# Performance work log

Hardware: AMD Instinct MI355X
Metric: run time of the kernel (lower is better)

Reference implementation:

```python
import jax, jax.numpy as jnp
import numpy as np

D_MODEL = 1024
NUM_HEADS = 16
D_K = D_MODEL // NUM_HEADS
B, L = 2, 4096


def setup_inputs() -> dict:
    key = jax.random.key(0)
    ks = jax.random.split(key, 12)
    s = 0.02
    return {
        "q": jax.random.normal(ks[0], (B, L, D_MODEL), dtype=jnp.float32),
        "k": jax.random.normal(ks[1], (B, L, D_MODEL), dtype=jnp.float32),
        "v": jax.random.normal(ks[2], (B, L, D_MODEL), dtype=jnp.float32),
        "Wq": jax.random.normal(ks[3], (D_MODEL, D_MODEL), dtype=jnp.float32) * s,
        "bq": jax.random.normal(ks[4], (D_MODEL,), dtype=jnp.float32) * s,
        "Wk": jax.random.normal(ks[5], (D_MODEL, D_MODEL), dtype=jnp.float32) * s,
        "bk": jax.random.normal(ks[6], (D_MODEL,), dtype=jnp.float32) * s,
        "Wv": jax.random.normal(ks[7], (D_MODEL, D_MODEL), dtype=jnp.float32) * s,
        "bv": jax.random.normal(ks[8], (D_MODEL,), dtype=jnp.float32) * s,
        "Wo": jax.random.normal(ks[9], (D_MODEL, D_MODEL), dtype=jnp.float32) * s,
        "bo": jax.random.normal(ks[10], (D_MODEL,), dtype=jnp.float32) * s,
    }


def reference(q, k, v, Wq, bq, Wk, bk, Wv, bv, Wo, bo):
    b, l, _ = q.shape
    # projections (torch Linear: x @ W.T + b), reshape to [b, l, h, d]
    qf = (q @ Wq.T + bq).reshape(b, l, NUM_HEADS, D_K)
    kf = (k @ Wk.T + bk).reshape(b, l, NUM_HEADS, D_K)
    vf = (v @ Wv.T + bv).reshape(b, l, NUM_HEADS, D_K)
    # elu+1 feature map (positive features)
    qf = jax.nn.elu(qf) + 1.0
    kf = jax.nn.elu(kf) + 1.0
    # normalizer uses full-sequence k sum (as in the original code)
    z = 1.0 / (jnp.einsum("blhd,bhd->blh", qf, kf.sum(axis=1)) + 1e-6)
    # cumulative sums over sequence (the linear-attention scan state)
    k_cum = jnp.cumsum(kf, axis=1)  # [b, l, h, d]
    v_cum = jnp.cumsum(vf, axis=1)  # [b, l, h, d]
    context = jnp.einsum("blhd,blhd->blh", qf, k_cum)  # [b, l, h]
    context = context[..., None] * v_cum * z[..., None]  # [b, l, h, d]
    context = context.reshape(b, l, NUM_HEADS * D_K)
    return context @ Wo.T + bo
```

## Files before the change

### kernel.cpp

```cpp
#include <hip/hip_runtime.h>
#include <hip/hip_bf16.h>
#include <cstdint>
#include <cstddef>

#define D_MODEL 1024
#define NUM_HEADS 16
#define DK_DIM 64
#define BATCH 2
#define SEQ 4096
#define MROWS (BATCH*SEQ)
#define NCHUNK 128
#define CHUNK 32

#define BM 256
#define BN 128
#define BK 64
#define NSLOT 3
#define SLOT_SH (BM*BK + BN*BK)
#define KTILES (D_MODEL/BK)

typedef __attribute__((ext_vector_type(4))) float f32x4;
typedef __attribute__((ext_vector_type(2))) float f32x2;
typedef __attribute__((ext_vector_type(8))) short bf16x8;
typedef __attribute__((ext_vector_type(4))) short s16x4;

__device__ __forceinline__ float b2f(short s) {
  union { uint32_t u; float f; } c; c.u = ((uint32_t)(uint16_t)s) << 16; return c.f;
}
__device__ __forceinline__ short f2b(float f) {
  union { float f; uint32_t u; } c; c.f = f;
  uint32_t u = c.u;
  u += 0x7FFFu + ((u >> 16) & 1u);
  return (short)(u >> 16);
}
__device__ __forceinline__ f32x4 b4_to_f4(s16x4 s) {
  f32x4 r;
  r.x = b2f(s.x); r.y = b2f(s.y); r.z = b2f(s.z); r.w = b2f(s.w);
  return r;
}

__global__ __launch_bounds__(256) void cvt_f32_bf16(const float* __restrict__ in,
                                                    short* __restrict__ out, int n4) {
  int i = blockIdx.x * 256 + threadIdx.x;
  if (i >= n4) return;
  float4 v = reinterpret_cast<const float4*>(in)[i];
  s16x4 o;
  o.x = f2b(v.x); o.y = f2b(v.y); o.z = f2b(v.z); o.w = f2b(v.w);
  reinterpret_cast<s16x4*>(out)[i] = o;
}

__global__ __launch_bounds__(256) void cvt_w4(
    const float* __restrict__ s0, const float* __restrict__ s1,
    const float* __restrict__ s2, const float* __restrict__ s3,
    short* __restrict__ dst) {
  const int y = blockIdx.y;
  const float* s = (y == 0) ? s0 : (y == 1) ? s1 : (y == 2) ? s2 : s3;
  const int i = blockIdx.x * 256 + threadIdx.x;
  float4 v = reinterpret_cast<const float4*>(s)[i];
  s16x4 o;
  o.x = f2b(v.x); o.y = f2b(v.y); o.z = f2b(v.z); o.w = f2b(v.w);
  reinterpret_cast<s16x4*>(dst)[(size_t)y * (D_MODEL * D_MODEL / 4) + i] = o;
}

template<int OUTBF16>
__global__ __launch_bounds__(512, 2) void gemm8(
    const short* __restrict__ A, const short* __restrict__ Bw,
    const float* __restrict__ bias, void* __restrict__ Cout, int act)
{
  extern __shared__ __align__(16) short lds[];
  const int tid = threadIdx.x;
  const int wid = tid >> 6;
  const int lane = tid & 63;
  const int brow = blockIdx.x * BM;
  const int bcol = blockIdx.y * BN;
  const int wr = wid >> 1, wc = wid & 1;

  f32x4 acc[4][4];
#pragma unroll
  for (int i = 0; i < 4; ++i)
#pragma unroll
    for (int j = 0; j < 4; ++j)
#pragma unroll
      for (int t = 0; t < 4; ++t) acc[i][j][t] = 0.f;

  const int srow = lane >> 3;
  const int sgel = ((lane & 7) ^ srow) * 8;

  auto stage = [&](int t) {
    short* sA = lds + (t % NSLOT) * SLOT_SH;
    short* sB = sA + BM * BK;
    const int k0 = t * BK;
#pragma unroll
    for (int i = 0; i < 4; ++i) {
      const int r = i * 64 + wid * 8;
      const short* g = A + (size_t)(brow + r + srow) * D_MODEL + k0 + sgel;
      __builtin_amdgcn_global_load_lds((const __attribute__((address_space(1))) void*)g,
          (__attribute__((address_space(3))) void*)(sA + r * BK), 16, 0, 0);
    }
#pragma unroll
    for (int i = 0; i < 2; ++i) {
      const int r = i * 64 + wid * 8;
      const short* g = Bw + (size_t)(bcol + r + srow) * D_MODEL + k0 + sgel;
      __builtin_amdgcn_global_load_lds((const __attribute__((address_space(1))) void*)g,
          (__attribute__((address_space(3))) void*)(sB + r * BK), 16, 0, 0);
    }
  };

  stage(0);
  stage(1);

  const int lane15 = lane & 15;
  const int swz = (lane & 7) << 4;
  const int kq = (lane >> 4) * 16;

  for (int t = 0; t < KTILES; ++t) {
    if (t == KTILES - 1) { asm volatile("s_waitcnt vmcnt(0)" ::: "memory"); }
    else                 { asm volatile("s_waitcnt vmcnt(6)" ::: "memory"); }
    __builtin_amdgcn_s_barrier();
    __builtin_amdgcn_sched_barrier(0);
    if (t + 2 < KTILES) stage(t + 2);

    const char* sAb = (const char*)(lds + (t % NSLOT) * SLOT_SH);
    const char* sBb = sAb + BM * BK * 2;

    auto rdA = [&](int mi, int ks) -> bf16x8 {
      const int row = wr * 64 + mi * 16 + lane15;
      const int off = row * 128 + (((ks * 64 + kq)) ^ swz);
      return *reinterpret_cast<const bf16x8*>(sAb + off);
    };
    auto rdB = [&](int nj, int ks) -> bf16x8 {
      const int row = wc * 64 + nj * 16 + lane15;
      const int off = row * 128 + (((ks * 64 + kq)) ^ swz);
      return *reinterpret_cast<const bf16x8*>(sBb + off);
    };

    bf16x8 Af[2][2], Bf[2][2][2];

#pragma unroll
    for (int m2 = 0; m2 < 2; ++m2)
#pragma unroll
      for (int ks = 0; ks < 2; ++ks) Af[m2][ks] = rdA(m2, ks);
#pragma unroll
    for (int j2 = 0; j2 < 2; ++j2)
#pragma unroll
      for (int ks = 0; ks < 2; ++ks) Bf[0][j2][ks] = rdB(j2, ks);
    __builtin_amdgcn_s_setprio(1);
#pragma unroll
    for (int m2 = 0; m2 < 2; ++m2)
#pragma unroll
      for (int j2 = 0; j2 < 2; ++j2)
#pragma unroll
        for (int ks = 0; ks < 2; ++ks)
          acc[m2][j2] = __builtin_amdgcn_mfma_f32_16x16x32_bf16(Af[m2][ks], Bf[0][j2][ks], acc[m2][j2], 0, 0, 0);
    __builtin_amdgcn_s_setprio(0);
    __builtin_amdgcn_sched_barrier(0);

#pragma unroll
    for (int j2 = 0; j2 < 2; ++j2)
#pragma unroll
      for (int ks = 0; ks < 2; ++ks) Bf[1][j2][ks] = rdB(2 + j2, ks);
    __builtin_amdgcn_s_setprio(1);
#pragma unroll
    for (int m2 = 0; m2 < 2; ++m2)
#pragma unroll
      for (int j2 = 0; j2 < 2; ++j2)
#pragma unroll
        for (int ks = 0; ks < 2; ++ks)
          acc[m2][2 + j2] = __builtin_amdgcn_mfma_f32_16x16x32_bf16(Af[m2][ks], Bf[1][j2][ks], acc[m2][2 + j2], 0, 0, 0);
    __builtin_amdgcn_s_setprio(0);
    __builtin_amdgcn_sched_barrier(0);

#pragma unroll
    for (int m2 = 0; m2 < 2; ++m2)
#pragma unroll
      for (int ks = 0; ks < 2; ++ks) Af[m2][ks] = rdA(2 + m2, ks);
    __builtin_amdgcn_s_setprio(1);
#pragma unroll
    for (int m2 = 0; m2 < 2; ++m2)
#pragma unroll
      for (int j2 = 0; j2 < 2; ++j2)
#pragma unroll
        for (int ks = 0; ks < 2; ++ks)
          acc[2 + m2][2 + j2] = __builtin_amdgcn_mfma_f32_16x16x32_bf16(Af[m2][ks], Bf[1][j2][ks], acc[2 + m2][2 + j2], 0, 0, 0);
    __builtin_amdgcn_s_setprio(0);
    __builtin_amdgcn_sched_barrier(0);

    __builtin_amdgcn_s_setprio(1);
#pragma unroll
    for (int m2 = 0; m2 < 2; ++m2)
#pragma unroll
      for (int j2 = 0; j2 < 2; ++j2)
#pragma unroll
        for (int ks = 0; ks < 2; ++ks)
          acc[2 + m2][j2] = __builtin_amdgcn_mfma_f32_16x16x32_bf16(Af[m2][ks], Bf[0][j2][ks], acc[2 + m2][j2], 0, 0, 0);
    __builtin_amdgcn_s_setprio(0);
    __builtin_amdgcn_sched_barrier(0);
  }

  const int rsub = (lane >> 4) * 4;
#pragma unroll
  for (int nj = 0; nj < 4; ++nj) {
    const int col = bcol + wc * 64 + nj * 16 + lane15;
    const float bv = bias[col];
#pragma unroll
    for (int mi = 0; mi < 4; ++mi) {
#pragma unroll
      for (int tt = 0; tt < 4; ++tt) {
        const int row = brow + wr * 64 + mi * 16 + rsub + tt;
        float v = acc[mi][nj][tt] + bv;
        if (act) v = (v > 0.f) ? (v + 1.f) : __expf(v);
        if (OUTBF16) ((short*)Cout)[(size_t)row * D_MODEL + col] = f2b(v);
        else ((float*)Cout)[(size_t)row * D_MODEL + col] = v;
      }
    }
  }
}

__global__ __launch_bounds__(256) void chunk_sums(
    const short* __restrict__ kf, const short* __restrict__ vf,
    float* __restrict__ ck, float* __restrict__ cv)
{
  const int gw = blockIdx.x * 4 + (threadIdx.x >> 6);
  const int lane = threadIdx.x & 63;
  const int c = gw & (NCHUNK - 1);
  const int h = (gw >> 7) & (NUM_HEADS - 1);
  const int b = gw >> 11;
  const int half = lane >> 5;
  const int dpair = (lane & 31) * 2;
  const size_t base = ((size_t)(b * SEQ + c * CHUNK) * NUM_HEADS + h) * DK_DIM + dpair;

  float skx = 0.f, sky = 0.f, svx = 0.f, svy = 0.f;
#pragma unroll
  for (int i = 0; i < CHUNK / 2; ++i) {
    const size_t off = base + (size_t)(2 * i + half) * D_MODEL;
    uint32_t ku = *reinterpret_cast<const uint32_t*>(&kf[off]);
    uint32_t vu = *reinterpret_cast<const uint32_t*>(&vf[off]);
    skx += b2f((short)(ku & 0xffff)); sky += b2f((short)(ku >> 16));
    svx += b2f((short)(vu & 0xffff)); svy += b2f((short)(vu >> 16));
  }
  skx += __shfl_xor(skx, 32, 64); sky += __shfl_xor(sky, 32, 64);
  svx += __shfl_xor(svx, 32, 64); svy += __shfl_xor(svy, 32, 64);
  if (half == 0) {
    const size_t o = ((size_t)((b * NUM_HEADS + h) * NCHUNK + c)) * DK_DIM + dpair;
    f32x2 a; a.x = skx; a.y = sky;
    f32x2 bb; bb.x = svx; bb.y = svy;
    *reinterpret_cast<f32x2*>(&ck[o]) = a;
    *reinterpret_cast<f32x2*>(&cv[o]) = bb;
  }
}

__global__ __launch_bounds__(64) void chunk_scan(
    float* __restrict__ ck, float* __restrict__ cv, float* __restrict__ ksum)
{
  const int bh = blockIdx.x;
  const int d = threadIdx.x;
  float rk = 0.f, rv = 0.f;
#pragma unroll 8
  for (int c = 0; c < NCHUNK; ++c) {
    const size_t o = ((size_t)(bh * NCHUNK + c)) * DK_DIM + d;
    const float tk = ck[o], tv = cv[o];
    ck[o] = rk; cv[o] = rv;
    rk += tk; rv += tv;
  }
  ksum[bh * DK_DIM + d] = rk;
}

__global__ __launch_bounds__(256) void scan_ctx(
    const short* __restrict__ qf, const short* __restrict__ kf,
    const short* __restrict__ vf,
    const float* __restrict__ ck, const float* __restrict__ cv,
    const float* __restrict__ ksum, short* __restrict__ ctx)
{
  const int gw = blockIdx.x * 4 + (threadIdx.x >> 6);
  const int lane = threadIdx.x & 63;
  const int pg = lane >> 4;
  const int dg = lane & 15;
  const int c = gw & (NCHUNK - 1);
  const int h = (gw >> 7) & (NUM_HEADS - 1);
  const int b = gw >> 11;
  const int bh = b * NUM_HEADS + h;
  const int d4 = dg * 4;

  f32x4 krun = *reinterpret_cast<const f32x4*>(
      &ck[((size_t)(bh * NCHUNK + c)) * DK_DIM + d4]);
  f32x4 vrun = *reinterpret_cast<const f32x4*>(
      &cv[((size_t)(bh * NCHUNK + c)) * DK_DIM + d4]);
  const f32x4 kst = *reinterpret_cast<const f32x4*>(&ksum[bh * DK_DIM + d4]);

  const size_t base = ((size_t)(b * SEQ + c * CHUNK) * NUM_HEADS + h) * DK_DIM + d4;

  for (int p0 = 0; p0 < CHUNK; p0 += 4) {
    const size_t qoff = base + (size_t)(p0 + pg) * D_MODEL;
    const f32x4 q4 = b4_to_f4(*reinterpret_cast<const s16x4*>(&qf[qoff]));
    f32x4 sk, sv;
#pragma unroll
    for (int i = 0; i < 4; ++i) {
      const size_t off = base + (size_t)(p0 + i) * D_MODEL;
      krun += b4_to_f4(*reinterpret_cast<const s16x4*>(&kf[off]));
      vrun += b4_to_f4(*reinterpret_cast<const s16x4*>(&vf[off]));
      if (i == pg) { sk = krun; sv = vrun; }
    }
    float s1 = q4.x * sk.x + q4.y * sk.y + q4.z * sk.z + q4.w * sk.w;
    float s2 = q4.x * kst.x + q4.y * kst.y + q4.z * kst.z + q4.w * kst.w;
#pragma unroll
    for (int m = 1; m < 16; m <<= 1) {
      s1 += __shfl_xor(s1, m, 64);
      s2 += __shfl_xor(s2, m, 64);
    }
    const float g = s1 / (s2 + 1e-6f);
    s16x4 o;
    o.x = f2b(g * sv.x); o.y = f2b(g * sv.y);
    o.z = f2b(g * sv.z); o.w = f2b(g * sv.w);
    *reinterpret_cast<s16x4*>(&ctx[qoff]) = o;
  }
}

extern "C" void kernel_launch(void* const* d_in, const int* in_sizes, int n_in,
                              void* d_out, int out_size, void* d_ws, size_t ws_size,
                              hipStream_t stream) {
  const float* q  = (const float*)d_in[0];
  const float* k  = (const float*)d_in[1];
  const float* v  = (const float*)d_in[2];
  const float* Wq = (const float*)d_in[3];
  const float* bq = (const float*)d_in[4];
  const float* Wk = (const float*)d_in[5];
  const float* bk = (const float*)d_in[6];
  const float* Wv = (const float*)d_in[7];
  const float* bv = (const float*)d_in[8];
  const float* Wo = (const float*)d_in[9];
  const float* bo = (const float*)d_in[10];
  float* out = (float*)d_out;

  uint8_t* p = (uint8_t*)d_ws;
  auto alloc = [&](size_t bytes) { uint8_t* r = p; p += bytes; return r; };
  short* inb = (short*)alloc((size_t)MROWS * D_MODEL * 2);
  short* qf  = (short*)alloc((size_t)MROWS * D_MODEL * 2);
  short* kf  = (short*)alloc((size_t)MROWS * D_MODEL * 2);
  short* vf  = (short*)alloc((size_t)MROWS * D_MODEL * 2);
  short* Wqb = (short*)alloc((size_t)D_MODEL * D_MODEL * 2);
  short* Wkb = (short*)alloc((size_t)D_MODEL * D_MODEL * 2);
  short* Wvb = (short*)alloc((size_t)D_MODEL * D_MODEL * 2);
  short* Wob = (short*)alloc((size_t)D_MODEL * D_MODEL * 2);
  float* ck   = (float*)alloc((size_t)BATCH * NUM_HEADS * NCHUNK * DK_DIM * 4);
  float* cv   = (float*)alloc((size_t)BATCH * NUM_HEADS * NCHUNK * DK_DIM * 4);
  float* ksum = (float*)alloc((size_t)BATCH * NUM_HEADS * DK_DIM * 4);
  short* ctx = inb;

  const int n4in = MROWS * D_MODEL / 4;
  const dim3 ggrid(MROWS / BM, D_MODEL / BN);
  const int shbytes = NSLOT * SLOT_SH * (int)sizeof(short);

  (void)hipFuncSetAttribute((const void*)gemm8<1>,
      hipFuncAttributeMaxDynamicSharedMemorySize, shbytes);
  (void)hipFuncSetAttribute((const void*)gemm8<0>,
      hipFuncAttributeMaxDynamicSharedMemorySize, shbytes);

  cvt_w4<<<dim3(D_MODEL * D_MODEL / 4 / 256, 4), 256, 0, stream>>>(Wq, Wk, Wv, Wo, Wqb);

  cvt_f32_bf16<<<n4in / 256, 256, 0, stream>>>(q, inb, n4in);
  gemm8<1><<<ggrid, 512, shbytes, stream>>>(inb, Wqb, bq, qf, 1);
  cvt_f32_bf16<<<n4in / 256, 256, 0, stream>>>(k, inb, n4in);
  gemm8<1><<<ggrid, 512, shbytes, stream>>>(inb, Wkb, bk, kf, 1);
  cvt_f32_bf16<<<n4in / 256, 256, 0, stream>>>(v, inb, n4in);
  gemm8<1><<<ggrid, 512, shbytes, stream>>>(inb, Wvb, bv, vf, 0);

  chunk_sums<<<BATCH * NUM_HEADS * NCHUNK / 4, 256, 0, stream>>>(kf, vf, ck, cv);
  chunk_scan<<<BATCH * NUM_HEADS, 64, 0, stream>>>(ck, cv, ksum);
  scan_ctx<<<BATCH * NUM_HEADS * NCHUNK / 4, 256, 0, stream>>>(qf, kf, vf, ck, cv, ksum, ctx);

  gemm8<0><<<ggrid, 512, shbytes, stream>>>(ctx, Wob, bo, out, 0);
}
```

Measured before the change: 154.6 us.

## Fuse fp32-to-bf16 input conversion into projection GEMM A-tile loading

Removes the three standalone fp32→bf16 conversion kernels for q/k/v. The projection GEMM now loads fp32 A tiles into registers, converts them with packed bf16 instructions and writes them to swizzled LDS in a register-double-buffered pipeline. It also swaps the MFMA operands so each lane holds four consecutive columns, which allows vectorized bias loads and vectorized output stores. This saves a full write and re-read of the bf16 inputs, at the cost of more register pressure and a manual LDS write path in the main loop.

Result: faster. 144.3 us (-6.7%).

```diff
diff --git a/kernel.cpp b/kernel.cpp
--- a/kernel.cpp
+++ b/kernel.cpp
@@ -23,6 +23,8 @@
 typedef __attribute__((ext_vector_type(2))) float f32x2;
 typedef __attribute__((ext_vector_type(8))) short bf16x8;
 typedef __attribute__((ext_vector_type(4))) short s16x4;
+typedef __attribute__((ext_vector_type(2))) uint32_t u32x2;
+typedef __attribute__((ext_vector_type(4))) uint32_t u32x4;
 
 __device__ __forceinline__ float b2f(short s) {
   union { uint32_t u; float f; } c; c.u = ((uint32_t)(uint16_t)s) << 16; return c.f;
@@ -38,15 +40,10 @@
   r.x = b2f(s.x); r.y = b2f(s.y); r.z = b2f(s.z); r.w = b2f(s.w);
   return r;
 }
-
-__global__ __launch_bounds__(256) void cvt_f32_bf16(const float* __restrict__ in,
-                                                    short* __restrict__ out, int n4) {
-  int i = blockIdx.x * 256 + threadIdx.x;
-  if (i >= n4) return;
-  float4 v = reinterpret_cast<const float4*>(in)[i];
-  s16x4 o;
-  o.x = f2b(v.x); o.y = f2b(v.y); o.z = f2b(v.z); o.w = f2b(v.w);
-  reinterpret_cast<s16x4*>(out)[i] = o;
+__device__ __forceinline__ uint32_t cvtpk(float lo, float hi) {
+  uint32_t r;
+  asm("v_cvt_pk_bf16_f32 %0, %1, %2" : "=v"(r) : "v"(lo), "v"(hi));
+  return r;
 }
 
 __global__ __launch_bounds__(256) void cvt_w4(
@@ -62,9 +59,9 @@
   reinterpret_cast<s16x4*>(dst)[(size_t)y * (D_MODEL * D_MODEL / 4) + i] = o;
 }
 
-template<int OUTBF16>
+template<int AFP32, int OUTBF16>
 __global__ __launch_bounds__(512, 2) void gemm8(
-    const short* __restrict__ A, const short* __restrict__ Bw,
+    const void* __restrict__ Ap, const short* __restrict__ Bw,
     const float* __restrict__ bias, void* __restrict__ Cout, int act)
 {
   extern __shared__ __align__(16) short lds[];
@@ -74,6 +71,8 @@
   const int brow = blockIdx.x * BM;
   const int bcol = blockIdx.y * BN;
   const int wr = wid >> 1, wc = wid & 1;
+  const float* __restrict__ A32 = (const float*)Ap;
+  const short* __restrict__ A16 = (const short*)Ap;
 
   f32x4 acc[4][4];
 #pragma unroll
@@ -84,19 +83,12 @@
       for (int t = 0; t < 4; ++t) acc[i][j][t] = 0.f;
 
   const int srow = lane >> 3;
-  const int sgel = ((lane & 7) ^ srow) * 8;
-
-  auto stage = [&](int t) {
-    short* sA = lds + (t % NSLOT) * SLOT_SH;
-    short* sB = sA + BM * BK;
+  const int gql  = lane & 7;
+  const int sgel = (gql ^ srow) * 8;
+
+  auto stageB = [&](int t) {
+    short* sB = lds + (t % NSLOT) * SLOT_SH + BM * BK;
     const int k0 = t * BK;
-#pragma unroll
-    for (int i = 0; i < 4; ++i) {
-      const int r = i * 64 + wid * 8;
-      const short* g = A + (size_t)(brow + r + srow) * D_MODEL + k0 + sgel;
-      __builtin_amdgcn_global_load_lds((const __attribute__((address_space(1))) void*)g,
-          (__attribute__((address_space(3))) void*)(sA + r * BK), 16, 0, 0);
-    }
 #pragma unroll
     for (int i = 0; i < 2; ++i) {
       const int r = i * 64 + wid * 8;
@@ -105,37 +97,58 @@
           (__attribute__((address_space(3))) void*)(sB + r * BK), 16, 0, 0);
     }
   };
-
-  stage(0);
-  stage(1);
+  auto stageA16 = [&](int t) {
+    short* sA = lds + (t % NSLOT) * SLOT_SH;
+    const int k0 = t * BK;
+#pragma unroll
+    for (int i = 0; i < 4; ++i) {
+      const int r = i * 64 + wid * 8;
+      const short* g = A16 + (size_t)(brow + r + srow) * D_MODEL + k0 + sgel;
+      __builtin_amdgcn_global_load_lds((const __attribute__((address_space(1))) void*)g,
+          (__attribute__((address_space(3))) void*)(sA + r * BK), 16, 0, 0);
+    }
+  };
+  auto loadA32 = [&](int t, float4 (&buf)[8]) {
+    const int k0 = t * BK;
+#pragma unroll
+    for (int i = 0; i < 4; ++i) {
+      const float* src = A32 + (size_t)(brow + i * 64 + wid * 8 + srow) * D_MODEL + k0 + gql * 8;
+      buf[2 * i]     = *reinterpret_cast<const float4*>(src);
+      buf[2 * i + 1] = *reinterpret_cast<const float4*>(src + 4);
+    }
+  };
+  auto writeA32 = [&](int t, float4 (&buf)[8]) {
+    char* sA = (char*)(lds + (t % NSLOT) * SLOT_SH);
+#pragma unroll
+    for (int i = 0; i < 4; ++i) {
+      u32x4 w;
+      w.x = cvtpk(buf[2 * i].x,     buf[2 * i].y);
+      w.y = cvtpk(buf[2 * i].z,     buf[2 * i].w);
+      w.z = cvtpk(buf[2 * i + 1].x, buf[2 * i + 1].y);
+      w.w = cvtpk(buf[2 * i + 1].z, buf[2 * i + 1].w);
+      const int ebyte = (i * 64 + wid * 8 + srow) * 128 + ((gql ^ srow) * 16);
+      *reinterpret_cast<u32x4*>(sA + ebyte) = w;
+    }
+  };
 
   const int lane15 = lane & 15;
   const int swz = (lane & 7) << 4;
   const int kq = (lane >> 4) * 16;
 
-  for (int t = 0; t < KTILES; ++t) {
-    if (t == KTILES - 1) { asm volatile("s_waitcnt vmcnt(0)" ::: "memory"); }
-    else                 { asm volatile("s_waitcnt vmcnt(6)" ::: "memory"); }
-    __builtin_amdgcn_s_barrier();
-    __builtin_amdgcn_sched_barrier(0);
-    if (t + 2 < KTILES) stage(t + 2);
-
+  auto compute = [&](int t) {
     const char* sAb = (const char*)(lds + (t % NSLOT) * SLOT_SH);
     const char* sBb = sAb + BM * BK * 2;
-
     auto rdA = [&](int mi, int ks) -> bf16x8 {
       const int row = wr * 64 + mi * 16 + lane15;
-      const int off = row * 128 + (((ks * 64 + kq)) ^ swz);
+      const int off = row * 128 + ((ks * 64 + kq) ^ swz);
       return *reinterpret_cast<const bf16x8*>(sAb + off);
     };
     auto rdB = [&](int nj, int ks) -> bf16x8 {
       const int row = wc * 64 + nj * 16 + lane15;
-      const int off = row * 128 + (((ks * 64 + kq)) ^ swz);
+      const int off = row * 128 + ((ks * 64 + kq) ^ swz);
       return *reinterpret_cast<const bf16x8*>(sBb + off);
     };
-
     bf16x8 Af[2][2], Bf[2][2][2];
-
 #pragma unroll
     for (int m2 = 0; m2 < 2; ++m2)
 #pragma unroll
@@ -151,10 +164,9 @@
       for (int j2 = 0; j2 < 2; ++j2)
 #pragma unroll
         for (int ks = 0; ks < 2; ++ks)
-          acc[m2][j2] = __builtin_amdgcn_mfma_f32_16x16x32_bf16(Af[m2][ks], Bf[0][j2][ks], acc[m2][j2], 0, 0, 0);
+          acc[m2][j2] = __builtin_amdgcn_mfma_f32_16x16x32_bf16(Bf[0][j2][ks], Af[m2][ks], acc[m2][j2], 0, 0, 0);
     __builtin_amdgcn_s_setprio(0);
     __builtin_amdgcn_sched_barrier(0);
-
 #pragma unroll
     for (int j2 = 0; j2 < 2; ++j2)
 #pragma unroll
@@ -166,10 +178,9 @@
       for (int j2 = 0; j2 < 2; ++j2)
 #pragma unroll
         for (int ks = 0; ks < 2; ++ks)
-          acc[m2][2 + j2] = __builtin_amdgcn_mfma_f32_16x16x32_bf16(Af[m2][ks], Bf[1][j2][ks], acc[m2][2 + j2], 0, 0, 0);
+          acc[m2][2 + j2] = __builtin_amdgcn_mfma_f32_16x16x32_bf16(Bf[1][j2][ks], Af[m2][ks], acc[m2][2 + j2], 0, 0, 0);
     __builtin_amdgcn_s_setprio(0);
     __builtin_amdgcn_sched_barrier(0);
-
 #pragma unroll
     for (int m2 = 0; m2 < 2; ++m2)
 #pragma unroll
@@ -181,10 +192,9 @@
       for (int j2 = 0; j2 < 2; ++j2)
 #pragma unroll
         for (int ks = 0; ks < 2; ++ks)
-          acc[2 + m2][2 + j2] = __builtin_amdgcn_mfma_f32_16x16x32_bf16(Af[m2][ks], Bf[1][j2][ks], acc[2 + m2][2 + j2], 0, 0, 0);
+          acc[2 + m2][2 + j2] = __builtin_amdgcn_mfma_f32_16x16x32_bf16(Bf[1][j2][ks], Af[m2][ks], acc[2 + m2][2 + j2], 0, 0, 0);
     __builtin_amdgcn_s_setprio(0);
     __builtin_amdgcn_sched_barrier(0);
-
     __builtin_amdgcn_s_setprio(1);
 #pragma unroll
     for (int m2 = 0; m2 < 2; ++m2)
@@ -192,25 +202,76 @@
       for (int j2 = 0; j2 < 2; ++j2)
 #pragma unroll
         for (int ks = 0; ks < 2; ++ks)
-          acc[2 + m2][j2] = __builtin_amdgcn_mfma_f32_16x16x32_bf16(Af[m2][ks], Bf[0][j2][ks], acc[2 + m2][j2], 0, 0, 0);
+          acc[2 + m2][j2] = __builtin_amdgcn_mfma_f32_16x16x32_bf16(Bf[0][j2][ks], Af[m2][ks], acc[2 + m2][j2], 0, 0, 0);
     __builtin_amdgcn_s_setprio(0);
     __builtin_amdgcn_sched_barrier(0);
-  }
-
-  const int rsub = (lane >> 4) * 4;
-#pragma unroll
-  for (int nj = 0; nj < 4; ++nj) {
-    const int col = bcol + wc * 64 + nj * 16 + lane15;
-    const float bv = bias[col];
-#pragma unroll
-    for (int mi = 0; mi < 4; ++mi) {
-#pragma unroll
-      for (int tt = 0; tt < 4; ++tt) {
-        const int row = brow + wr * 64 + mi * 16 + rsub + tt;
-        float v = acc[mi][nj][tt] + bv;
-        if (act) v = (v > 0.f) ? (v + 1.f) : __expf(v);
-        if (OUTBF16) ((short*)Cout)[(size_t)row * D_MODEL + col] = f2b(v);
-        else ((float*)Cout)[(size_t)row * D_MODEL + col] = v;
+  };
+
+  if constexpr (AFP32) {
+    float4 buf0[8], buf1[8];
+    loadA32(0, buf0);
+    asm volatile("s_waitcnt vmcnt(0)" ::: "memory");
+    writeA32(0, buf0);
+    loadA32(1, buf1);
+    stageB(0); stageB(1);
+
+    auto body = [&](int t, float4 (&bufW)[8], float4 (&bufL)[8]) {
+      if (t == KTILES - 1) { asm volatile("s_waitcnt vmcnt(0)" ::: "memory"); }
+      else                 { asm volatile("s_waitcnt vmcnt(2)" ::: "memory"); }
+      if (t + 1 < KTILES) writeA32(t + 1, bufW);
+      if (t + 2 < KTILES) loadA32(t + 2, bufL);
+      asm volatile("s_waitcnt lgkmcnt(0)" ::: "memory");
+      __builtin_amdgcn_s_barrier();
+      __builtin_amdgcn_sched_barrier(0);
+      if (t + 2 < KTILES) stageB(t + 2);
+      compute(t);
+    };
+#pragma unroll 1
+    for (int t2 = 0; t2 < KTILES; t2 += 2) {
+      body(t2,     buf1, buf0);
+      body(t2 + 1, buf0, buf1);
+    }
+  } else {
+    stageA16(0); stageB(0);
+    stageA16(1); stageB(1);
+#pragma unroll 1
+    for (int t = 0; t < KTILES; ++t) {
+      if (t == KTILES - 1) { asm volatile("s_waitcnt vmcnt(0)" ::: "memory"); }
+      else                 { asm volatile("s_waitcnt vmcnt(6)" ::: "memory"); }
+      __builtin_amdgcn_s_barrier();
+      __builtin_amdgcn_sched_barrier(0);
+      if (t + 2 < KTILES) { stageA16(t + 2); stageB(t + 2); }
+      compute(t);
+    }
+  }
+
+  const int csub4 = (lane >> 4) * 4;
+#pragma unroll
+  for (int mi = 0; mi < 4; ++mi) {
+    const int row = brow + wr * 64 + mi * 16 + lane15;
+    const size_t rowbase = (size_t)row * D_MODEL;
+#pragma unroll
+    for (int nj = 0; nj < 4; ++nj) {
+      const int col0 = bcol + wc * 64 + nj * 16 + csub4;
+      const float4 bv = *reinterpret_cast<const float4*>(&bias[col0]);
+      float v0 = acc[mi][nj][0] + bv.x;
+      float v1 = acc[mi][nj][1] + bv.y;
+      float v2 = acc[mi][nj][2] + bv.z;
+      float v3 = acc[mi][nj][3] + bv.w;
+      if (act) {
+        v0 = (v0 > 0.f) ? (v0 + 1.f) : __expf(v0);
+        v1 = (v1 > 0.f) ? (v1 + 1.f) : __expf(v1);
+        v2 = (v2 > 0.f) ? (v2 + 1.f) : __expf(v2);
+        v3 = (v3 > 0.f) ? (v3 + 1.f) : __expf(v3);
+      }
+      if (OUTBF16) {
+        u32x2 w;
+        w.x = cvtpk(v0, v1);
+        w.y = cvtpk(v2, v3);
+        *reinterpret_cast<u32x2*>(&((short*)Cout)[rowbase + col0]) = w;
+      } else {
+        float4 w; w.x = v0; w.y = v1; w.z = v2; w.w = v3;
+        *reinterpret_cast<float4*>(&((float*)Cout)[rowbase + col0]) = w;
       }
     }
   }
@@ -333,10 +394,10 @@
 
   uint8_t* p = (uint8_t*)d_ws;
   auto alloc = [&](size_t bytes) { uint8_t* r = p; p += bytes; return r; };
-  short* inb = (short*)alloc((size_t)MROWS * D_MODEL * 2);
   short* qf  = (short*)alloc((size_t)MROWS * D_MODEL * 2);
   short* kf  = (short*)alloc((size_t)MROWS * D_MODEL * 2);
   short* vf  = (short*)alloc((size_t)MROWS * D_MODEL * 2);
+  short* ctx = (short*)alloc((size_t)MROWS * D_MODEL * 2);
   short* Wqb = (short*)alloc((size_t)D_MODEL * D_MODEL * 2);
   short* Wkb = (short*)alloc((size_t)D_MODEL * D_MODEL * 2);
   short* Wvb = (short*)alloc((size_t)D_MODEL * D_MODEL * 2);
@@ -344,29 +405,24 @@
   float* ck   = (float*)alloc((size_t)BATCH * NUM_HEADS * NCHUNK * DK_DIM * 4);
   float* cv   = (float*)alloc((size_t)BATCH * NUM_HEADS * NCHUNK * DK_DIM * 4);
   float* ksum = (float*)alloc((size_t)BATCH * NUM_HEADS * DK_DIM * 4);
-  short* ctx = inb;
-
-  const int n4in = MROWS * D_MODEL / 4;
+
   const dim3 ggrid(MROWS / BM, D_MODEL / BN);
   const int shbytes = NSLOT * SLOT_SH * (int)sizeof(short);
 
-  (void)hipFuncSetAttribute((const void*)gemm8<1>,
+  (void)hipFuncSetAttribute((const void*)gemm8<1, 1>,
       hipFuncAttributeMaxDynamicSharedMemorySize, shbytes);
-  (void)hipFuncSetAttribute((const void*)gemm8<0>,
+  (void)hipFuncSetAttribute((const void*)gemm8<0, 0>,
       hipFuncAttributeMaxDynamicSharedMemorySize, shbytes);
 
   cvt_w4<<<dim3(D_MODEL * D_MODEL / 4 / 256, 4), 256, 0, stream>>>(Wq, Wk, Wv, Wo, Wqb);
 
-  cvt_f32_bf16<<<n4in / 256, 256, 0, stream>>>(q, inb, n4in);
-  gemm8<1><<<ggrid, 512, shbytes, stream>>>(inb, Wqb, bq, qf, 1);
-  cvt_f32_bf16<<<n4in / 256, 256, 0, stream>>>(k, inb, n4in);
-  gemm8<1><<<ggrid, 512, shbytes, stream>>>(inb, Wkb, bk, kf, 1);
-  cvt_f32_bf16<<<n4in / 256, 256, 0, stream>>>(v, inb, n4in);
-  gemm8<1><<<ggrid, 512, shbytes, stream>>>(inb, Wvb, bv, vf, 0);
+  gemm8<1, 1><<<ggrid, 512, shbytes, stream>>>(q, Wqb, bq, qf, 1);
+  gemm8<1, 1><<<ggrid, 512, shbytes, stream>>>(k, Wkb, bk, kf, 1);
+  gemm8<1, 1><<<ggrid, 512, shbytes, stream>>>(v, Wvb, bv, vf, 0);
 
   chunk_sums<<<BATCH * NUM_HEADS * NCHUNK / 4, 256, 0, stream>>>(kf, vf, ck, cv);
   chunk_scan<<<BATCH * NUM_HEADS, 64, 0, stream>>>(ck, cv, ksum);
   scan_ctx<<<BATCH * NUM_HEADS * NCHUNK / 4, 256, 0, stream>>>(qf, kf, vf, ck, cv, ksum, ctx);
 
-  gemm8<0><<<ggrid, 512, shbytes, stream>>>(ctx, Wob, bo, out, 0);
-}
+  gemm8<0, 0><<<ggrid, 512, shbytes, stream>>>(ctx, Wob, bo, out, 0);
+}
```
